# Kernel optimization log

Measured on AMD Instinct MI355X. Metric: run time of the kernel, lower is better.

The kernel has to match this reference:

```python
import jax, jax.numpy as jnp
import numpy as np

N, D, HID, ATT, B, NC = 131072, 1024, 256, 128, 64, 2
EPS = 1e-5

def _ln(h, g, b):
    mu = jnp.mean(h, axis=-1, keepdims=True)
    var = jnp.mean((h - mu) ** 2, axis=-1, keepdims=True)
    return (h - mu) * jax.lax.rsqrt(var + EPS) * g + b

def _gelu(x):
    return jax.nn.gelu(x, approximate=False)  # torch nn.GELU default (erf)

def setup_inputs() -> dict:
    key = jax.random.key(0)
    ks = jax.random.split(key, 16)
    def w(k, shape, fan_in):
        return (jax.random.normal(k, shape, jnp.float32) / np.sqrt(fan_in)).astype(jnp.float32)
    # sorted, every bag non-empty (~equal sizes)
    segment_ids = ((jnp.arange(N) * B) // N).astype(jnp.int32)
    return {
        "x": jax.random.normal(ks[0], (N, D), jnp.float32),
        "segment_ids": segment_ids,
        "W1": w(ks[1], (D, HID), D), "b1": jnp.zeros((HID,), jnp.float32),
        "g1": jnp.ones((HID,), jnp.float32), "be1": jnp.zeros((HID,), jnp.float32),
        "W2": w(ks[2], (HID, HID), HID), "b2": jnp.zeros((HID,), jnp.float32),
        "g2": jnp.ones((HID,), jnp.float32), "be2": jnp.zeros((HID,), jnp.float32),
        "Wv": w(ks[3], (HID, ATT), HID), "bv": jnp.zeros((ATT,), jnp.float32),
        "Wu": w(ks[4], (HID, ATT), HID), "bu": jnp.zeros((ATT,), jnp.float32),
        "Ww": w(ks[5], (ATT, 1), ATT), "bw": jnp.zeros((1,), jnp.float32),
        "Wc1": w(ks[6], (HID, HID // 2), HID), "bc1": jnp.zeros((HID // 2,), jnp.float32),
        "Wc2": w(ks[7], (HID // 2, NC), HID // 2), "bc2": jnp.zeros((NC,), jnp.float32),
    }

def reference(x, segment_ids, W1, b1, g1, be1, W2, b2, g2, be2,
              Wv, bv, Wu, bu, Ww, bw, Wc1, bc1, Wc2, bc2):
    # encoder (dropout = identity at inference)
    h = _gelu(_ln(x @ W1 + b1, g1, be1))          # [N, HID]
    h = _gelu(_ln(h @ W2 + b2, g2, be2))          # [N, HID]
    # gated attention logits
    a = (jnp.tanh(h @ Wv + bv) * jax.nn.sigmoid(h @ Wu + bu)) @ Ww + bw  # [N, 1]
    a = a[:, 0]                                    # [N]
    # per-bag (segment) softmax
    m = jax.ops.segment_max(a, segment_ids, num_segments=B)             # [B]
    e = jnp.exp(a - m[segment_ids])
    s = jax.ops.segment_sum(e, segment_ids, num_segments=B)             # [B]
    attn = e / s[segment_ids]                                           # [N]
    # attention-weighted bag pooling
    z = jax.ops.segment_sum(attn[:, None] * h, segment_ids, num_segments=B)  # [B, HID]
    # classifier
    logits = _gelu(z @ Wc1 + bc1) @ Wc2 + bc2       # [B, NC]
    return logits
```

## Files before the change

kernel.cpp:

```cpp
#include <hip/hip_runtime.h>
#include <math.h>

#define N_TOK  131072
#define DIM    1024
#define HIDN   256
#define ATTN   128
#define NSEG   64
#define SEGLEN 2048
#define NCLS   2
#define EPSLN  1e-5f

typedef __attribute__((ext_vector_type(8))) short  short8;
typedef __attribute__((ext_vector_type(4))) float  f32x4;

__device__ __forceinline__ unsigned short f2bf(float f) {
    unsigned int u = __float_as_uint(f);
    u += 0x7fffu + ((u >> 16) & 1u);
    return (unsigned short)(u >> 16);
}
__device__ __forceinline__ float bf2f(unsigned short h) {
    return __uint_as_float(((unsigned int)h) << 16);
}
__device__ __forceinline__ float gelu_exact(float x) {
    return 0.5f * x * (1.0f + erff(x * 0.70710678118654752f));
}

__global__ __launch_bounds__(256) void transpose_cvt(const float* __restrict__ in,
                                                     unsigned short* __restrict__ out,
                                                     int R, int C) {
    __shared__ float t[32][33];
    const int bx = blockIdx.x * 32;
    const int by = blockIdx.y * 32;
    const int x = threadIdx.x, y = threadIdx.y;
#pragma unroll
    for (int i = 0; i < 32; i += 8) {
        int r = by + y + i, c = bx + x;
        if (r < R && c < C) t[y + i][x] = in[(size_t)r * C + c];
    }
    __syncthreads();
#pragma unroll
    for (int i = 0; i < 32; i += 8) {
        int c = bx + y + i, r = by + x;
        if (c < C && r < R) out[(size_t)c * R + r] = f2bf(t[x][y + i]);
    }
}

__global__ void build_bvu(const float* __restrict__ bv, const float* __restrict__ bu,
                          float* __restrict__ bvu) {
    int t = threadIdx.x;
    bvu[t] = (t < 128) ? bv[t] : bu[t - 128];
}

template <int K, int MODE, bool AF32>
__global__ __launch_bounds__(256) void gemm_fused(const void* __restrict__ Aptr,
                                                  const unsigned short* __restrict__ Wt,
                                                  const float* __restrict__ bias,
                                                  const float* __restrict__ g,
                                                  const float* __restrict__ be,
                                                  unsigned short* __restrict__ Hout,
                                                  const float* __restrict__ Ww,
                                                  const float* __restrict__ bw,
                                                  float* __restrict__ Aout) {
    constexpr int SMEM_BYTES = (MODE == 1) ? 33536 : 25600;
    __shared__ __align__(16) char smem[SMEM_BYTES];
    auto As = (unsigned short (*)[40])(smem);
    auto Ws = (unsigned short (*)[40])(smem + 5120);

    const int tid  = threadIdx.x;
    const int wave = tid >> 6, lane = tid & 63;
    const int lr = lane & 15, lq = lane >> 4;
    const int srow = tid >> 2, skq = (tid & 3) * 8;
    const size_t row0 = (size_t)blockIdx.x * 64;

    f32x4 acc[4][4];
#pragma unroll
    for (int i = 0; i < 4; i++)
#pragma unroll
        for (int j = 0; j < 4; j++) acc[i][j] = (f32x4)0.0f;

    for (int k0 = 0; k0 < K; k0 += 32) {
        short8 aw;
        if constexpr (AF32) {
            const float* A = (const float*)Aptr;
            const float* p = &A[(row0 + srow) * K + k0 + skq];
            float4 v0 = *(const float4*)p;
            float4 v1 = *(const float4*)(p + 4);
            aw[0] = (short)f2bf(v0.x); aw[1] = (short)f2bf(v0.y);
            aw[2] = (short)f2bf(v0.z); aw[3] = (short)f2bf(v0.w);
            aw[4] = (short)f2bf(v1.x); aw[5] = (short)f2bf(v1.y);
            aw[6] = (short)f2bf(v1.z); aw[7] = (short)f2bf(v1.w);
        } else {
            const unsigned short* A = (const unsigned short*)Aptr;
            aw = *(const short8*)&A[(row0 + srow) * K + k0 + skq];
        }
        short8 ww[4];
#pragma unroll
        for (int c = 0; c < 4; c++)
            ww[c] = *(const short8*)&Wt[(size_t)(srow + 64 * c) * K + k0 + skq];

        __syncthreads();
        *(short8*)&As[srow][skq] = aw;
#pragma unroll
        for (int c = 0; c < 4; c++)
            *(short8*)&Ws[srow + 64 * c][skq] = ww[c];
        __syncthreads();

        short8 a[4], b[4];
#pragma unroll
        for (int i = 0; i < 4; i++) a[i] = *(const short8*)&As[16 * i + lr][lq * 8];
#pragma unroll
        for (int j = 0; j < 4; j++) b[j] = *(const short8*)&Ws[64 * wave + 16 * j + lr][lq * 8];
#pragma unroll
        for (int i = 0; i < 4; i++)
#pragma unroll
            for (int j = 0; j < 4; j++)
                acc[i][j] = __builtin_amdgcn_mfma_f32_16x16x32_bf16(a[i], b[j], acc[i][j], 0, 0, 0);
    }

    __syncthreads();

    float bjv[4];
#pragma unroll
    for (int j = 0; j < 4; j++) bjv[j] = bias[wave * 64 + 16 * j + lr];
#pragma unroll
    for (int i = 0; i < 4; i++)
#pragma unroll
        for (int j = 0; j < 4; j++)
#pragma unroll
            for (int r = 0; r < 4; r++) acc[i][j][r] += bjv[j];

    if constexpr (MODE == 0) {
        float (*red)[4][64] = (float (*)[4][64])smem;
#pragma unroll
        for (int i = 0; i < 4; i++)
#pragma unroll
            for (int r = 0; r < 4; r++) {
                float s = 0.0f, sq = 0.0f;
#pragma unroll
                for (int j = 0; j < 4; j++) { float v = acc[i][j][r]; s += v; sq += v * v; }
#pragma unroll
                for (int m = 1; m < 16; m <<= 1) { s += __shfl_xor(s, m); sq += __shfl_xor(sq, m); }
                if (lr == 0) {
                    red[0][wave][16 * i + 4 * lq + r] = s;
                    red[1][wave][16 * i + 4 * lq + r] = sq;
                }
            }
        __syncthreads();
        float gj[4], bej[4];
#pragma unroll
        for (int j = 0; j < 4; j++) {
            gj[j]  = g[wave * 64 + 16 * j + lr];
            bej[j] = be[wave * 64 + 16 * j + lr];
        }
#pragma unroll
        for (int i = 0; i < 4; i++)
#pragma unroll
            for (int r = 0; r < 4; r++) {
                const int row = 16 * i + 4 * lq + r;
                const float s  = red[0][0][row] + red[0][1][row] + red[0][2][row] + red[0][3][row];
                const float sq = red[1][0][row] + red[1][1][row] + red[1][2][row] + red[1][3][row];
                const float mu  = s * (1.0f / HIDN);
                const float var = sq * (1.0f / HIDN) - mu * mu;
                const float rs  = rsqrtf(var + EPSLN);
#pragma unroll
                for (int j = 0; j < 4; j++) {
                    const float o = (acc[i][j][r] - mu) * rs * gj[j] + bej[j];
                    Hout[(row0 + row) * 256 + wave * 64 + 16 * j + lr] = f2bf(gelu_exact(o));
                }
            }
    } else {
        float (*us)[129] = (float (*)[129])smem;
        float (*pw)[64]  = (float (*)[64])(smem + 33024);
        if (wave >= 2) {
            const int cb = (wave - 2) * 64;
#pragma unroll
            for (int i = 0; i < 4; i++)
#pragma unroll
                for (int j = 0; j < 4; j++)
#pragma unroll
                    for (int r = 0; r < 4; r++)
                        us[16 * i + 4 * lq + r][cb + 16 * j + lr] =
                            1.0f / (1.0f + expf(-acc[i][j][r]));
        }
        __syncthreads();
        if (wave < 2) {
            const int cb = wave * 64;
            float wwj[4];
#pragma unroll
            for (int j = 0; j < 4; j++) wwj[j] = Ww[cb + 16 * j + lr];
#pragma unroll
            for (int i = 0; i < 4; i++)
#pragma unroll
                for (int r = 0; r < 4; r++) {
                    const int row = 16 * i + 4 * lq + r;
                    float s = 0.0f;
#pragma unroll
                    for (int j = 0; j < 4; j++)
                        s += tanhf(acc[i][j][r]) * us[row][cb + 16 * j + lr] * wwj[j];
#pragma unroll
                    for (int m = 1; m < 16; m <<= 1) s += __shfl_xor(s, m);
                    if (lr == 0) pw[wave][row] = s;
                }
        }
        __syncthreads();
        if (tid < 64) Aout[row0 + tid] = pw[0][tid] + pw[1][tid] + bw[0];
    }
}

__global__ __launch_bounds__(256) void seg_softmax(float* __restrict__ A) {
    __shared__ float red[256];
    const int seg = blockIdx.x, tid = threadIdx.x;
    float* a = A + (size_t)seg * SEGLEN;
    float m = -1e30f;
#pragma unroll
    for (int c = 0; c < 8; c++) m = fmaxf(m, a[tid + 256 * c]);
    red[tid] = m; __syncthreads();
    for (int s = 128; s > 0; s >>= 1) {
        if (tid < s) red[tid] = fmaxf(red[tid], red[tid + s]);
        __syncthreads();
    }
    m = red[0]; __syncthreads();
    float e[8]; float sum = 0.0f;
#pragma unroll
    for (int c = 0; c < 8; c++) { e[c] = expf(a[tid + 256 * c] - m); sum += e[c]; }
    red[tid] = sum; __syncthreads();
    for (int s = 128; s > 0; s >>= 1) {
        if (tid < s) red[tid] += red[tid + s];
        __syncthreads();
    }
    const float inv = 1.0f / red[0];
#pragma unroll
    for (int c = 0; c < 8; c++) a[tid + 256 * c] = e[c] * inv;
}

__global__ __launch_bounds__(256) void pool_partial(const float* __restrict__ Attn,
                                                    const unsigned short* __restrict__ H,
                                                    float* __restrict__ Zp) {
    __shared__ float aw[256];
    const int tid = threadIdx.x;
    const size_t rbase = (size_t)blockIdx.x * 256;
    aw[tid] = Attn[rbase + tid];
    __syncthreads();
    const unsigned short* h = H + rbase * 256 + tid;
    float acc = 0.0f;
    for (int r = 0; r < 256; r++) acc += aw[r] * bf2f(h[(size_t)r * 256]);
    Zp[rbase + tid] = acc;
}

__global__ __launch_bounds__(256) void head_kernel(const float* __restrict__ Zp,
                                                   const float* __restrict__ Wc1,
                                                   const float* __restrict__ bc1,
                                                   const float* __restrict__ Wc2,
                                                   const float* __restrict__ bc2,
                                                   float* __restrict__ Out) {
    __shared__ float zs[256];
    __shared__ float hs[128];
    __shared__ float red[4];
    const int seg = blockIdx.x, tid = threadIdx.x;
    float z = 0.0f;
#pragma unroll
    for (int c = 0; c < 8; c++) z += Zp[((size_t)seg * 8 + c) * 256 + tid];
    zs[tid] = z;
    __syncthreads();
    if (tid < 128) {
        float acc = bc1[tid];
        for (int k = 0; k < 256; k++) acc += zs[k] * Wc1[k * 128 + tid];
        hs[tid] = gelu_exact(acc);
    }
    __syncthreads();
    const int cls = tid >> 7, j = tid & 127;
    float val = hs[j] * Wc2[j * 2 + cls];
#pragma unroll
    for (int o = 32; o > 0; o >>= 1) val += __shfl_down(val, o);
    if ((tid & 63) == 0) red[tid >> 6] = val;
    __syncthreads();
    if (tid < 2) Out[seg * 2 + tid] = red[tid * 2] + red[tid * 2 + 1] + bc2[tid];
}

extern "C" void kernel_launch(void* const* d_in, const int* in_sizes, int n_in,
                              void* d_out, int out_size, void* d_ws, size_t ws_size,
                              hipStream_t stream) {
    const float* x   = (const float*)d_in[0];
    const float* W1  = (const float*)d_in[2];
    const float* b1  = (const float*)d_in[3];
    const float* g1  = (const float*)d_in[4];
    const float* be1 = (const float*)d_in[5];
    const float* W2  = (const float*)d_in[6];
    const float* b2  = (const float*)d_in[7];
    const float* g2  = (const float*)d_in[8];
    const float* be2 = (const float*)d_in[9];
    const float* Wv  = (const float*)d_in[10];
    const float* bv  = (const float*)d_in[11];
    const float* Wu  = (const float*)d_in[12];
    const float* bu  = (const float*)d_in[13];
    const float* Ww  = (const float*)d_in[14];
    const float* bw  = (const float*)d_in[15];
    const float* Wc1 = (const float*)d_in[16];
    const float* bc1 = (const float*)d_in[17];
    const float* Wc2 = (const float*)d_in[18];
    const float* bc2 = (const float*)d_in[19];
    float* out = (float*)d_out;

    char* p = (char*)d_ws;
    unsigned short* h1b    = (unsigned short*)p; p += (size_t)N_TOK * HIDN * 2;
    unsigned short* h2b    = (unsigned short*)p; p += (size_t)N_TOK * HIDN * 2;
    float*          scores = (float*)p;          p += (size_t)N_TOK * 4;
    unsigned short* W1t    = (unsigned short*)p; p += (size_t)HIDN * DIM * 2;
    unsigned short* W2t    = (unsigned short*)p; p += (size_t)HIDN * HIDN * 2;
    unsigned short* Wvut   = (unsigned short*)p; p += (size_t)HIDN * HIDN * 2;
    float*          bvu    = (float*)p;          p += 256 * 4;
    float*          Zp     = (float*)p;          p += (size_t)NSEG * 8 * HIDN * 4;

    dim3 tb(32, 8);
    transpose_cvt<<<dim3(HIDN / 32, DIM / 32), tb, 0, stream>>>(W1, W1t, DIM, HIDN);
    transpose_cvt<<<dim3(HIDN / 32, HIDN / 32), tb, 0, stream>>>(W2, W2t, HIDN, HIDN);
    transpose_cvt<<<dim3(ATTN / 32, HIDN / 32), tb, 0, stream>>>(Wv, Wvut, HIDN, ATTN);
    transpose_cvt<<<dim3(ATTN / 32, HIDN / 32), tb, 0, stream>>>(Wu, Wvut + (size_t)ATTN * HIDN, HIDN, ATTN);
    build_bvu<<<1, 256, 0, stream>>>(bv, bu, bvu);

    gemm_fused<DIM, 0, true><<<N_TOK / 64, 256, 0, stream>>>(
        x, W1t, b1, g1, be1, h1b, nullptr, nullptr, nullptr);
    gemm_fused<HIDN, 0, false><<<N_TOK / 64, 256, 0, stream>>>(
        h1b, W2t, b2, g2, be2, h2b, nullptr, nullptr, nullptr);
    gemm_fused<HIDN, 1, false><<<N_TOK / 64, 256, 0, stream>>>(
        h2b, Wvut, bvu, nullptr, nullptr, nullptr, Ww, bw, scores);

    seg_softmax<<<NSEG, 256, 0, stream>>>(scores);
    pool_partial<<<NSEG * 8, 256, 0, stream>>>(scores, h2b, Zp);
    head_kernel<<<NSEG, 256, 0, stream>>>(Zp, Wc1, bc1, Wc2, bc2, out);
}
```

Baseline: 1.008 ms.

## Double-buffer GEMM LDS tiles and vectorize pooling loads

The fused GEMM kernel now uses two LDS tile buffers. The global loads for the next K-tile are issued before the MFMA work on the current tile, which removes one barrier per iteration and overlaps memory latency with compute. LDS grows to 50KB and the launch bounds ask for 3 waves per SIMD, which may cap registers or occupancy. The pooling kernel now reads 8 bf16 values per thread with vector loads across row groups and reduces the partial sums in shared memory, replacing the per-thread strided scalar loads.

```diff
diff --git a/kernel.cpp b/kernel.cpp
--- a/kernel.cpp
+++ b/kernel.cpp
@@ -52,19 +52,21 @@
 }
 
 template <int K, int MODE, bool AF32>
-__global__ __launch_bounds__(256) void gemm_fused(const void* __restrict__ Aptr,
-                                                  const unsigned short* __restrict__ Wt,
-                                                  const float* __restrict__ bias,
-                                                  const float* __restrict__ g,
-                                                  const float* __restrict__ be,
-                                                  unsigned short* __restrict__ Hout,
-                                                  const float* __restrict__ Ww,
-                                                  const float* __restrict__ bw,
-                                                  float* __restrict__ Aout) {
-    constexpr int SMEM_BYTES = (MODE == 1) ? 33536 : 25600;
-    __shared__ __align__(16) char smem[SMEM_BYTES];
-    auto As = (unsigned short (*)[40])(smem);
-    auto Ws = (unsigned short (*)[40])(smem + 5120);
+__global__ __launch_bounds__(256, 3) void gemm_fused(const void* __restrict__ Aptr,
+                                                     const unsigned short* __restrict__ Wt,
+                                                     const float* __restrict__ bias,
+                                                     const float* __restrict__ g,
+                                                     const float* __restrict__ be,
+                                                     unsigned short* __restrict__ Hout,
+                                                     const float* __restrict__ Ww,
+                                                     const float* __restrict__ bw,
+                                                     float* __restrict__ Aout) {
+    constexpr int NT = K / 32;
+    __shared__ __align__(16) char smem[51200];
+    auto As0 = (unsigned short (*)[40])(smem);
+    auto As1 = (unsigned short (*)[40])(smem + 5120);
+    auto Ws0 = (unsigned short (*)[40])(smem + 10240);
+    auto Ws1 = (unsigned short (*)[40])(smem + 10240 + 20480);
 
     const int tid  = threadIdx.x;
     const int wave = tid >> 6, lane = tid & 63;
@@ -78,8 +80,7 @@
 #pragma unroll
         for (int j = 0; j < 4; j++) acc[i][j] = (f32x4)0.0f;
 
-    for (int k0 = 0; k0 < K; k0 += 32) {
-        short8 aw;
+    auto loadA = [&](int k0, short8& aw) {
         if constexpr (AF32) {
             const float* A = (const float*)Aptr;
             const float* p = &A[(row0 + srow) * K + k0 + skq];
@@ -93,18 +94,20 @@
             const unsigned short* A = (const unsigned short*)Aptr;
             aw = *(const short8*)&A[(row0 + srow) * K + k0 + skq];
         }
-        short8 ww[4];
+    };
+    auto loadW = [&](int k0, short8* ww) {
 #pragma unroll
         for (int c = 0; c < 4; c++)
             ww[c] = *(const short8*)&Wt[(size_t)(srow + 64 * c) * K + k0 + skq];
-
-        __syncthreads();
+    };
+    auto writeT = [&](unsigned short (*As)[40], unsigned short (*Ws)[40],
+                      const short8& aw, const short8* ww) {
         *(short8*)&As[srow][skq] = aw;
 #pragma unroll
         for (int c = 0; c < 4; c++)
             *(short8*)&Ws[srow + 64 * c][skq] = ww[c];
-        __syncthreads();
-
+    };
+    auto mmaT = [&](unsigned short (*As)[40], unsigned short (*Ws)[40]) {
         short8 a[4], b[4];
 #pragma unroll
         for (int i = 0; i < 4; i++) a[i] = *(const short8*)&As[16 * i + lr][lq * 8];
@@ -115,9 +118,29 @@
 #pragma unroll
             for (int j = 0; j < 4; j++)
                 acc[i][j] = __builtin_amdgcn_mfma_f32_16x16x32_bf16(a[i], b[j], acc[i][j], 0, 0, 0);
-    }
-
-    __syncthreads();
+    };
+
+    short8 aw;
+    short8 ww[4];
+    loadA(0, aw);
+    loadW(0, ww);
+    writeT(As0, Ws0, aw, ww);
+    __syncthreads();
+
+    for (int t = 0; t < NT; t += 2) {
+        loadA(32 * (t + 1), aw);
+        loadW(32 * (t + 1), ww);
+        mmaT(As0, Ws0);
+        writeT(As1, Ws1, aw, ww);
+        __syncthreads();
+        if (t + 2 < NT) {
+            loadA(32 * (t + 2), aw);
+            loadW(32 * (t + 2), ww);
+        }
+        mmaT(As1, Ws1);
+        if (t + 2 < NT) writeT(As0, Ws0, aw, ww);
+        __syncthreads();
+    }
 
     float bjv[4];
 #pragma unroll
@@ -237,14 +260,29 @@
                                                     const unsigned short* __restrict__ H,
                                                     float* __restrict__ Zp) {
     __shared__ float aw[256];
+    __shared__ float part[8][256];
     const int tid = threadIdx.x;
     const size_t rbase = (size_t)blockIdx.x * 256;
     aw[tid] = Attn[rbase + tid];
     __syncthreads();
-    const unsigned short* h = H + rbase * 256 + tid;
-    float acc = 0.0f;
-    for (int r = 0; r < 256; r++) acc += aw[r] * bf2f(h[(size_t)r * 256]);
-    Zp[rbase + tid] = acc;
+    const int cg = tid & 31;
+    const int rg = tid >> 5;
+    float acc[8];
+#pragma unroll
+    for (int j = 0; j < 8; j++) acc[j] = 0.0f;
+    for (int r = rg * 32; r < rg * 32 + 32; ++r) {
+        short8 h8 = *(const short8*)&H[(rbase + r) * 256 + cg * 8];
+        const float a = aw[r];
+#pragma unroll
+        for (int j = 0; j < 8; j++) acc[j] += a * bf2f((unsigned short)h8[j]);
+    }
+#pragma unroll
+    for (int j = 0; j < 8; j++) part[rg][cg * 8 + j] = acc[j];
+    __syncthreads();
+    float s = 0.0f;
+#pragma unroll
+    for (int gq = 0; gq < 8; gq++) s += part[gq][tid];
+    Zp[rbase + tid] = s;
 }
 
 __global__ __launch_bounds__(256) void head_kernel(const float* __restrict__ Zp,
```

Result: no change. 1.007 ms (-0.1%).
